# Optimization experiments

Measured on AMD Instinct MI355X. Metric: run time of the kernel, lower is better.

## Reference

```python
import jax, jax.numpy as jnp
import numpy as np
from jax import lax

K = 7          # k1 = k2
L1 = 8
L2 = 8
BLK = 8        # block_size
DIV = 4        # histogram bin-merge factor from extract_features_big_memory
DN = ('NCHW', 'OIHW', 'NCHW')
PAD = [(K // 2, K // 2), (K // 2, K // 2)]


def setup_inputs() -> dict:
    key = jax.random.key(0)
    k1, k2, k3 = jax.random.split(key, 3)
    x = jax.random.normal(k1, (32, 3, 128, 128), dtype=jnp.float32)
    w1 = jax.random.normal(k2, (L1, 3, K, K), dtype=jnp.float32)   # l1_conv weight
    w2 = jax.random.normal(k3, (L2, 1, K, K), dtype=jnp.float32)   # l2_conv weight
    return {"x": x, "w1": w1, "w2": w2}


def reference(x, w1, w2):
    # ----- two PCA-filter convolutions (same padding, stride 1, no bias) -----
    out1 = lax.conv_general_dilated(x, w1, (1, 1), PAD, dimension_numbers=DN)
    num, ch, w, h = out1.shape                      # ch == L1
    out2 = lax.conv_general_dilated(out1.reshape(num * ch, 1, w, h), w2,
                                    (1, 1), PAD, dimension_numbers=DN)
    out2 = out2.reshape(num, ch, L2, w, h)

    # ----- heaviside + bit-pack to decimal codes in [0, 2^L2) -----
    bits = (out2 > 0).astype(jnp.int32)             # (num, L1, L2, w, h)
    weights = (2 ** jnp.arange(L2, dtype=jnp.int32))[None, None, :, None, None]
    decimal = jnp.sum(bits * weights, axis=2)       # (num, L1, w, h) integer codes

    # ----- non-overlapping BLKxBLK blocks (step == BLK, exact tiling) -----
    nb_w, nb_h = w // BLK, h // BLK
    blocks = decimal.reshape(num, ch, nb_w, BLK, nb_h, BLK)
    blocks = blocks.transpose(0, 1, 2, 4, 3, 5).reshape(num, ch, nb_w * nb_h, BLK * BLK)

    # ----- per-block histogram with 2^L2 / DIV coarse bins (width DIV) -----
    n_bins = (2 ** L2) // DIV                        # 64
    bucket = blocks // DIV                           # (num, ch, nblocks, BLK*BLK)
    flat = bucket.reshape(-1, BLK * BLK)             # (N, 64 pixels)
    N = flat.shape[0]
    counts = jnp.zeros((N, n_bins), jnp.float32).at[
        jnp.arange(N)[:, None], flat].add(1.0)       # scatter-add histogram
    return counts.reshape(num, -1)                   # (num, L1*nblocks*n_bins)
```

## Files before the change

kernel.cpp:

```cpp
#include <hip/hip_runtime.h>
#include <hip/hip_bf16.h>

#define KK 7
#define NL1 8
#define NL2 8
#define IMG 128
#define REG 32
#define RT 38
#define O1P 40
#define XR 44
#define XTP 44
#define NBINS 64
#define NHB 16


#define LDX12(dst, plane, row, col)                                          \
    { float4 t_;                                                             \
      t_ = *(const float4*)&xt[plane][row][col];                             \
      dst[0]=t_.x; dst[1]=t_.y; dst[2]=t_.z; dst[3]=t_.w;                    \
      t_ = *(const float4*)&xt[plane][row][(col)+4];                         \
      dst[4]=t_.x; dst[5]=t_.y; dst[6]=t_.z; dst[7]=t_.w;                    \
      t_ = *(const float4*)&xt[plane][row][(col)+8];                         \
      dst[8]=t_.x; dst[9]=t_.y; dst[10]=t_.z; dst[11]=t_.w; }

#define C1TAPS(acc0, acc1, acc2, acc3, dp)                                   \
    _Pragma("unroll")                                                        \
    for (int dq = 0; dq < KK; ++dq) {                                        \
        float wa = w1g[(dp) * 7 + dq];                                       \
        float wb = w1g[49 + (dp) * 7 + dq];                                  \
        float wc = w1g[98 + (dp) * 7 + dq];                                  \
        acc0 = __builtin_fmaf(f0[dq + 0], wa, acc0);                         \
        acc0 = __builtin_fmaf(f1[dq + 0], wb, acc0);                         \
        acc0 = __builtin_fmaf(f2[dq + 0], wc, acc0);                         \
        acc1 = __builtin_fmaf(f0[dq + 1], wa, acc1);                         \
        acc1 = __builtin_fmaf(f1[dq + 1], wb, acc1);                         \
        acc1 = __builtin_fmaf(f2[dq + 1], wc, acc1);                         \
        acc2 = __builtin_fmaf(f0[dq + 2], wa, acc2);                         \
        acc2 = __builtin_fmaf(f1[dq + 2], wb, acc2);                         \
        acc2 = __builtin_fmaf(f2[dq + 2], wc, acc2);                         \
        acc3 = __builtin_fmaf(f0[dq + 3], wa, acc3);                         \
        acc3 = __builtin_fmaf(f1[dq + 3], wb, acc3);                         \
        acc3 = __builtin_fmaf(f2[dq + 3], wc, acc3);                         \
    }

__global__ __launch_bounds__(256, 5) void pcanet_fused(
    const float* __restrict__ x,
    const float* __restrict__ w1,
    const float* __restrict__ w2,
    float* __restrict__ out)
{
    const int tid = threadIdx.x;
    const int reg = blockIdx.x;
    const int ch  = blockIdx.y;
    const int n   = blockIdx.z;
    const int P0  = (reg >> 2) * REG;
    const int Q0  = (reg & 3) * REG;

    __shared__ __align__(16) float xt[3][XR][XTP];
    __shared__ __align__(16) float o1[RT][O1P];
    __shared__ unsigned int hist[NHB * 32];

    const float* __restrict__ w1g = w1 + ch * 147;
    const float* __restrict__ w2g = w2;

    {
        const int lane = tid & 63;
        const int wv   = tid >> 6;
        const float* xn = x + (size_t)n * 3 * IMG * IMG;
        const int gs = Q0 - 6 + lane;
        const bool cok = (gs >= 0) && (gs < IMG);
        if (lane < XTP) {
            for (int c = 0; c < 3; ++c)
                for (int r = wv; r < XR; r += 4) {
                    int gr = P0 - 6 + r;
                    float v = 0.0f;
                    if (cok && gr >= 0 && gr < IMG)
                        v = xn[((size_t)c * IMG + gr) * IMG + gs];
                    xt[c][r][lane] = v;
                }
        }
    }
    for (int i = tid; i < NHB * 32; i += 256) hist[i] = 0u;
    __syncthreads();

    if (tid < 190) {
        int pr = tid / 10;
        int c1 = 4 * (tid % 10);
        int r0 = 2 * pr;
        float a0 = 0.f, a1 = 0.f, a2 = 0.f, a3 = 0.f;
        float b0 = 0.f, b1 = 0.f, b2 = 0.f, b3 = 0.f;
        #pragma unroll
        for (int e = 0; e < 8; ++e) {
            float f0[12], f1[12], f2[12];
            LDX12(f0, 0, r0 + e, c1)
            LDX12(f1, 1, r0 + e, c1)
            LDX12(f2, 2, r0 + e, c1)
            if (e < 7) { C1TAPS(a0, a1, a2, a3, e) }
            if (e >= 1) { C1TAPS(b0, b1, b2, b3, e - 1) }
        }
        int gs0 = Q0 - 3 + c1;
        bool c0ok = (gs0 + 0 >= 0 && gs0 + 0 < IMG);
        bool c1ok = (gs0 + 1 >= 0 && gs0 + 1 < IMG);
        bool c2ok = (gs0 + 2 >= 0 && gs0 + 2 < IMG);
        bool c3ok = (gs0 + 3 >= 0 && gs0 + 3 < IMG);
        {
            int gr = P0 - 3 + r0;
            bool rok = (gr >= 0 && gr < IMG);
            float4 st;
            st.x = (rok && c0ok) ? a0 : 0.f;
            st.y = (rok && c1ok) ? a1 : 0.f;
            st.z = (rok && c2ok) ? a2 : 0.f;
            st.w = (rok && c3ok) ? a3 : 0.f;
            *(float4*)&o1[r0][c1] = st;
        }
        {
            int gr = P0 - 3 + r0 + 1;
            bool rok = (gr >= 0 && gr < IMG);
            float4 st;
            st.x = (rok && c0ok) ? b0 : 0.f;
            st.y = (rok && c1ok) ? b1 : 0.f;
            st.z = (rok && c2ok) ? b2 : 0.f;
            st.w = (rok && c3ok) ? b3 : 0.f;
            *(float4*)&o1[r0 + 1][c1] = st;
        }
    }
    __syncthreads();

    {
        const int r  = tid >> 3;
        const int c0 = (tid & 7) * 4;
        float acc[NL2][4];
        #pragma unroll
        for (int l = 0; l < NL2; ++l)
            #pragma unroll
            for (int k = 0; k < 4; ++k) acc[l][k] = 0.f;

        for (int dp = 0; dp < KK; ++dp) {
            float f[12];
            { float4 t_;
              t_ = *(const float4*)&o1[r + dp][c0];
              f[0]=t_.x; f[1]=t_.y; f[2]=t_.z; f[3]=t_.w;
              t_ = *(const float4*)&o1[r + dp][c0 + 4];
              f[4]=t_.x; f[5]=t_.y; f[6]=t_.z; f[7]=t_.w;
              t_ = *(const float4*)&o1[r + dp][c0 + 8];
              f[8]=t_.x; f[9]=t_.y; f[10]=t_.z; f[11]=t_.w; }
            #pragma unroll
            for (int l = 0; l < NL2; ++l)
                #pragma unroll
                for (int dq = 0; dq < KK; ++dq) {
                    float w = w2g[l * 49 + dp * 7 + dq];
                    acc[l][0] = __builtin_fmaf(f[dq + 0], w, acc[l][0]);
                    acc[l][1] = __builtin_fmaf(f[dq + 1], w, acc[l][1]);
                    acc[l][2] = __builtin_fmaf(f[dq + 2], w, acc[l][2]);
                    acc[l][3] = __builtin_fmaf(f[dq + 3], w, acc[l][3]);
                }
        }
        #pragma unroll
        for (int k = 0; k < 4; ++k) {
            int code = 0;
            #pragma unroll
            for (int l = 0; l < NL2; ++l)
                if (acc[l][k] > 0.0f) code |= (1 << l);
            int bin = code >> 2;
            int bc = (c0 + k) >> 3, br = r >> 3;
            atomicAdd(&hist[(br * 4 + bc) * 32 + (bin >> 1)],
                      1u << (16 * (bin & 1)));
        }
    }
    __syncthreads();

    size_t planeBase = ((size_t)(n * NL1 + ch)) * 256 * NBINS;
    for (int i = tid; i < NHB * NBINS; i += 256) {
        int bl = i >> 6, bin = i & 63;
        unsigned int w = hist[bl * 32 + (bin >> 1)];
        unsigned int cnt = (w >> (16 * (bin & 1))) & 0xFFFFu;
        int br = bl >> 2, bc = bl & 3;
        int blkg = ((P0 >> 3) + br) * 16 + ((Q0 >> 3) + bc);
        out[planeBase + (size_t)blkg * NBINS + bin] = (float)cnt;
    }
}

extern "C" void kernel_launch(void* const* d_in, const int* in_sizes, int n_in,
                              void* d_out, int out_size, void* d_ws, size_t ws_size,
                              hipStream_t stream) {
    const float* x  = (const float*)d_in[0];
    const float* w1 = (const float*)d_in[1];
    const float* w2 = (const float*)d_in[2];
    float* out = (float*)d_out;

    dim3 grid(16, NL1, 32);
    dim3 block(256);
    pcanet_fused<<<grid, block, 0, stream>>>(x, w1, w2, out);
}
```

Measured before the change: 82.15 us.

## Make each wave compute its own conv1 stripe and histogram blocks, removing block barriers

The block is split so each wavefront computes the conv1 rows it needs for its own 8-row stripe, including the halo, then runs conv2 and its own 4 histogram blocks. This removes the two block-wide __syncthreads that separated the conv1, conv2 and histogram stages. In exchange, conv1 halo rows are computed redundantly by neighbouring waves. Each wave now runs two passes of conv1 tasks, and the second pass leaves most lanes idle.

New measurement: 113.5 us. +38.2%, slower.

```diff
diff --git a/kernel.cpp b/kernel.cpp
--- a/kernel.cpp
+++ b/kernel.cpp
@@ -49,7 +49,9 @@
     const float* __restrict__ w2,
     float* __restrict__ out)
 {
-    const int tid = threadIdx.x;
+    const int tid  = threadIdx.x;
+    const int wave = tid >> 6;
+    const int lane = tid & 63;
     const int reg = blockIdx.x;
     const int ch  = blockIdx.y;
     const int n   = blockIdx.z;
@@ -64,14 +66,12 @@
     const float* __restrict__ w2g = w2;
 
     {
-        const int lane = tid & 63;
-        const int wv   = tid >> 6;
         const float* xn = x + (size_t)n * 3 * IMG * IMG;
         const int gs = Q0 - 6 + lane;
         const bool cok = (gs >= 0) && (gs < IMG);
         if (lane < XTP) {
             for (int c = 0; c < 3; ++c)
-                for (int r = wv; r < XR; r += 4) {
+                for (int r = wave; r < XR; r += 4) {
                     int gr = P0 - 6 + r;
                     float v = 0.0f;
                     if (cok && gr >= 0 && gr < IMG)
@@ -80,55 +80,59 @@
                 }
         }
     }
-    for (int i = tid; i < NHB * 32; i += 256) hist[i] = 0u;
+    hist[wave * 128 + lane]      = 0u;
+    hist[wave * 128 + 64 + lane] = 0u;
     __syncthreads();
 
-    if (tid < 190) {
-        int pr = tid / 10;
-        int c1 = 4 * (tid % 10);
-        int r0 = 2 * pr;
-        float a0 = 0.f, a1 = 0.f, a2 = 0.f, a3 = 0.f;
-        float b0 = 0.f, b1 = 0.f, b2 = 0.f, b3 = 0.f;
-        #pragma unroll
-        for (int e = 0; e < 8; ++e) {
-            float f0[12], f1[12], f2[12];
-            LDX12(f0, 0, r0 + e, c1)
-            LDX12(f1, 1, r0 + e, c1)
-            LDX12(f2, 2, r0 + e, c1)
-            if (e < 7) { C1TAPS(a0, a1, a2, a3, e) }
-            if (e >= 1) { C1TAPS(b0, b1, b2, b3, e - 1) }
-        }
-        int gs0 = Q0 - 3 + c1;
-        bool c0ok = (gs0 + 0 >= 0 && gs0 + 0 < IMG);
-        bool c1ok = (gs0 + 1 >= 0 && gs0 + 1 < IMG);
-        bool c2ok = (gs0 + 2 >= 0 && gs0 + 2 < IMG);
-        bool c3ok = (gs0 + 3 >= 0 && gs0 + 3 < IMG);
-        {
-            int gr = P0 - 3 + r0;
-            bool rok = (gr >= 0 && gr < IMG);
-            float4 st;
-            st.x = (rok && c0ok) ? a0 : 0.f;
-            st.y = (rok && c1ok) ? a1 : 0.f;
-            st.z = (rok && c2ok) ? a2 : 0.f;
-            st.w = (rok && c3ok) ? a3 : 0.f;
-            *(float4*)&o1[r0][c1] = st;
-        }
-        {
-            int gr = P0 - 3 + r0 + 1;
-            bool rok = (gr >= 0 && gr < IMG);
-            float4 st;
-            st.x = (rok && c0ok) ? b0 : 0.f;
-            st.y = (rok && c1ok) ? b1 : 0.f;
-            st.z = (rok && c2ok) ? b2 : 0.f;
-            st.w = (rok && c3ok) ? b3 : 0.f;
-            *(float4*)&o1[r0 + 1][c1] = st;
+    #pragma unroll
+    for (int t = 0; t < 2; ++t) {
+        int task = lane + (t << 6);
+        if (task < 70) {
+            int pr = task / 10;
+            int c1 = 4 * (task % 10);
+            int r0 = (wave << 3) + 2 * pr;
+            float a0 = 0.f, a1 = 0.f, a2 = 0.f, a3 = 0.f;
+            float b0 = 0.f, b1 = 0.f, b2 = 0.f, b3 = 0.f;
+            #pragma unroll
+            for (int e = 0; e < 8; ++e) {
+                float f0[12], f1[12], f2[12];
+                LDX12(f0, 0, r0 + e, c1)
+                LDX12(f1, 1, r0 + e, c1)
+                LDX12(f2, 2, r0 + e, c1)
+                if (e < 7)  { C1TAPS(a0, a1, a2, a3, e) }
+                if (e >= 1) { C1TAPS(b0, b1, b2, b3, e - 1) }
+            }
+            int gs0 = Q0 - 3 + c1;
+            bool c0ok = (gs0 + 0 >= 0 && gs0 + 0 < IMG);
+            bool c1ok = (gs0 + 1 >= 0 && gs0 + 1 < IMG);
+            bool c2ok = (gs0 + 2 >= 0 && gs0 + 2 < IMG);
+            bool c3ok = (gs0 + 3 >= 0 && gs0 + 3 < IMG);
+            {
+                int gr = P0 - 3 + r0;
+                bool rok = (gr >= 0 && gr < IMG);
+                float4 st;
+                st.x = (rok && c0ok) ? a0 : 0.f;
+                st.y = (rok && c1ok) ? a1 : 0.f;
+                st.z = (rok && c2ok) ? a2 : 0.f;
+                st.w = (rok && c3ok) ? a3 : 0.f;
+                *(float4*)&o1[r0][c1] = st;
+            }
+            {
+                int gr = P0 - 3 + r0 + 1;
+                bool rok = (gr >= 0 && gr < IMG);
+                float4 st;
+                st.x = (rok && c0ok) ? b0 : 0.f;
+                st.y = (rok && c1ok) ? b1 : 0.f;
+                st.z = (rok && c2ok) ? b2 : 0.f;
+                st.w = (rok && c3ok) ? b3 : 0.f;
+                *(float4*)&o1[r0 + 1][c1] = st;
+            }
         }
     }
-    __syncthreads();
 
     {
-        const int r  = tid >> 3;
-        const int c0 = (tid & 7) * 4;
+        const int r  = (wave << 3) + (lane >> 3);
+        const int c0 = (lane & 7) * 4;
         float acc[NL2][4];
         #pragma unroll
         for (int l = 0; l < NL2; ++l)
@@ -162,16 +166,16 @@
             for (int l = 0; l < NL2; ++l)
                 if (acc[l][k] > 0.0f) code |= (1 << l);
             int bin = code >> 2;
-            int bc = (c0 + k) >> 3, br = r >> 3;
-            atomicAdd(&hist[(br * 4 + bc) * 32 + (bin >> 1)],
+            int blkid = (wave << 2) + ((c0 + k) >> 3);
+            atomicAdd(&hist[blkid * 32 + (bin >> 1)],
                       1u << (16 * (bin & 1)));
         }
     }
-    __syncthreads();
 
     size_t planeBase = ((size_t)(n * NL1 + ch)) * 256 * NBINS;
-    for (int i = tid; i < NHB * NBINS; i += 256) {
-        int bl = i >> 6, bin = i & 63;
+    for (int i = lane; i < 4 * NBINS; i += 64) {
+        int bl = (wave << 2) + (i >> 6);
+        int bin = i & 63;
         unsigned int w = hist[bl * 32 + (bin >> 1)];
         unsigned int cnt = (w >> (16 * (bin & 1))) & 0xFFFFu;
         int br = bl >> 2, bc = bl & 3;
```

## Split fused kernel into conv1-to-workspace and conv2-histogram kernels

Applied to the files above, without the earlier changes.

Replaces the single fused kernel with two launches when workspace allows. The first computes all 8 first-stage channels per tile once and writes them to global memory. The second reads one channel's halo tile from that buffer and does conv2 and the histogram. This removes the halo recompute and the 8x redundant conv1 work across channel blocks, at the cost of a 16MB global round trip and an extra launch. The old fused path is kept as a fallback.

Result: slower. 272.1 us (+231.2%).

```diff
diff --git a/kernel.cpp b/kernel.cpp
--- a/kernel.cpp
+++ b/kernel.cpp
@@ -23,29 +23,77 @@
       t_ = *(const float4*)&xt[plane][row][(col)+8];                         \
       dst[8]=t_.x; dst[9]=t_.y; dst[10]=t_.z; dst[11]=t_.w; }
 
-#define C1TAPS(acc0, acc1, acc2, acc3, dp)                                   \
-    _Pragma("unroll")                                                        \
-    for (int dq = 0; dq < KK; ++dq) {                                        \
-        float wa = w1g[(dp) * 7 + dq];                                       \
-        float wb = w1g[49 + (dp) * 7 + dq];                                  \
-        float wc = w1g[98 + (dp) * 7 + dq];                                  \
-        acc0 = __builtin_fmaf(f0[dq + 0], wa, acc0);                         \
-        acc0 = __builtin_fmaf(f1[dq + 0], wb, acc0);                         \
-        acc0 = __builtin_fmaf(f2[dq + 0], wc, acc0);                         \
-        acc1 = __builtin_fmaf(f0[dq + 1], wa, acc1);                         \
-        acc1 = __builtin_fmaf(f1[dq + 1], wb, acc1);                         \
-        acc1 = __builtin_fmaf(f2[dq + 1], wc, acc1);                         \
-        acc2 = __builtin_fmaf(f0[dq + 2], wa, acc2);                         \
-        acc2 = __builtin_fmaf(f1[dq + 2], wb, acc2);                         \
-        acc2 = __builtin_fmaf(f2[dq + 2], wc, acc2);                         \
-        acc3 = __builtin_fmaf(f0[dq + 3], wa, acc3);                         \
-        acc3 = __builtin_fmaf(f1[dq + 3], wb, acc3);                         \
-        acc3 = __builtin_fmaf(f2[dq + 3], wc, acc3);                         \
-    }
-
-__global__ __launch_bounds__(256, 5) void pcanet_fused(
+__global__ __launch_bounds__(256, 2) void pcanet_conv1(
     const float* __restrict__ x,
     const float* __restrict__ w1,
+    float* __restrict__ o1g)
+{
+    const int tid = threadIdx.x;
+    const int reg = blockIdx.x;
+    const int n   = blockIdx.y;
+    const int P0  = (reg >> 2) * REG;
+    const int Q0  = (reg & 3) * REG;
+
+    __shared__ __align__(16) float xt[3][RT][O1P];
+
+    {
+        const int lane = tid & 63, wv = tid >> 6;
+        const float* xn = x + (size_t)n * 3 * IMG * IMG;
+        const int gc = Q0 - 3 + lane;
+        const bool cok = (gc >= 0 && gc < IMG);
+        if (lane < O1P) {
+            for (int c = 0; c < 3; ++c)
+                for (int r = wv; r < RT; r += 4) {
+                    int gr = P0 - 3 + r;
+                    float v = 0.f;
+                    if (cok && gr >= 0 && gr < IMG)
+                        v = xn[((size_t)c * IMG + gr) * IMG + gc];
+                    xt[c][r][lane] = v;
+                }
+        }
+    }
+    __syncthreads();
+
+    const int row = tid >> 3;
+    const int c1  = (tid & 7) * 4;
+    float acc[NL1][4];
+    #pragma unroll
+    for (int ch = 0; ch < NL1; ++ch)
+        #pragma unroll
+        for (int k = 0; k < 4; ++k) acc[ch][k] = 0.f;
+
+    #pragma unroll
+    for (int e = 0; e < KK; ++e) {
+        float f0[12], f1[12], f2[12];
+        LDX12(f0, 0, row + e, c1)
+        LDX12(f1, 1, row + e, c1)
+        LDX12(f2, 2, row + e, c1)
+        #pragma unroll
+        for (int ch = 0; ch < NL1; ++ch)
+            #pragma unroll
+            for (int dq = 0; dq < KK; ++dq) {
+                const float wa = w1[ch * 147 +      e * 7 + dq];
+                const float wb = w1[ch * 147 + 49 + e * 7 + dq];
+                const float wc = w1[ch * 147 + 98 + e * 7 + dq];
+                #pragma unroll
+                for (int k = 0; k < 4; ++k) {
+                    acc[ch][k] = __builtin_fmaf(f0[dq + k], wa, acc[ch][k]);
+                    acc[ch][k] = __builtin_fmaf(f1[dq + k], wb, acc[ch][k]);
+                    acc[ch][k] = __builtin_fmaf(f2[dq + k], wc, acc[ch][k]);
+                }
+            }
+    }
+    const int gr = P0 + row, gc = Q0 + c1;
+    #pragma unroll
+    for (int ch = 0; ch < NL1; ++ch) {
+        float4 st;
+        st.x = acc[ch][0]; st.y = acc[ch][1]; st.z = acc[ch][2]; st.w = acc[ch][3];
+        *(float4*)&o1g[(((size_t)n * NL1 + ch) * IMG + gr) * IMG + gc] = st;
+    }
+}
+
+__global__ __launch_bounds__(256, 8) void pcanet_conv2(
+    const float* __restrict__ o1g,
     const float* __restrict__ w2,
     float* __restrict__ out)
 {
@@ -56,6 +104,123 @@
     const int P0  = (reg >> 2) * REG;
     const int Q0  = (reg & 3) * REG;
 
+    __shared__ __align__(16) float o1[RT][O1P];
+    __shared__ unsigned int hist[NHB * 32];
+
+    const float* __restrict__ w2g = w2;
+
+    {
+        const int lane = tid & 63, wv = tid >> 6;
+        const float* src = o1g + ((size_t)n * NL1 + ch) * IMG * IMG;
+        const int gc = Q0 - 3 + lane;
+        const bool cok = (gc >= 0 && gc < IMG);
+        if (lane < O1P) {
+            for (int r = wv; r < RT; r += 4) {
+                int gr = P0 - 3 + r;
+                float v = 0.f;
+                if (cok && gr >= 0 && gr < IMG)
+                    v = src[(size_t)gr * IMG + gc];
+                o1[r][lane] = v;
+            }
+        }
+    }
+    for (int i = tid; i < NHB * 32; i += 256) hist[i] = 0u;
+    __syncthreads();
+
+    {
+        const int r  = tid >> 3;
+        const int c0 = (tid & 7) * 4;
+        float acc[NL2][4];
+        #pragma unroll
+        for (int l = 0; l < NL2; ++l)
+            #pragma unroll
+            for (int k = 0; k < 4; ++k) acc[l][k] = 0.f;
+
+        for (int dp = 0; dp < KK; ++dp) {
+            float f[12];
+            { float4 t_;
+              t_ = *(const float4*)&o1[r + dp][c0];
+              f[0]=t_.x; f[1]=t_.y; f[2]=t_.z; f[3]=t_.w;
+              t_ = *(const float4*)&o1[r + dp][c0 + 4];
+              f[4]=t_.x; f[5]=t_.y; f[6]=t_.z; f[7]=t_.w;
+              t_ = *(const float4*)&o1[r + dp][c0 + 8];
+              f[8]=t_.x; f[9]=t_.y; f[10]=t_.z; f[11]=t_.w; }
+            #pragma unroll
+            for (int l = 0; l < NL2; ++l)
+                #pragma unroll
+                for (int dq = 0; dq < KK; ++dq) {
+                    float w = w2g[l * 49 + dp * 7 + dq];
+                    acc[l][0] = __builtin_fmaf(f[dq + 0], w, acc[l][0]);
+                    acc[l][1] = __builtin_fmaf(f[dq + 1], w, acc[l][1]);
+                    acc[l][2] = __builtin_fmaf(f[dq + 2], w, acc[l][2]);
+                    acc[l][3] = __builtin_fmaf(f[dq + 3], w, acc[l][3]);
+                }
+        }
+        #pragma unroll
+        for (int k = 0; k < 4; ++k) {
+            int code = 0;
+            #pragma unroll
+            for (int l = 0; l < NL2; ++l)
+                if (acc[l][k] > 0.0f) code |= (1 << l);
+            int bin = code >> 2;
+            int bc = (c0 + k) >> 3, br = r >> 3;
+            atomicAdd(&hist[(br * 4 + bc) * 32 + (bin >> 1)],
+                      1u << (16 * (bin & 1)));
+        }
+    }
+    __syncthreads();
+
+    size_t planeBase = ((size_t)(n * NL1 + ch)) * 256 * NBINS;
+    for (int i = tid; i < NHB * NBINS; i += 256) {
+        int bl = i >> 6, bin = i & 63;
+        unsigned int w = hist[bl * 32 + (bin >> 1)];
+        unsigned int cnt = (w >> (16 * (bin & 1))) & 0xFFFFu;
+        int br = bl >> 2, bc = bl & 3;
+        int blkg = ((P0 >> 3) + br) * 16 + ((Q0 >> 3) + bc);
+        out[planeBase + (size_t)blkg * NBINS + bin] = (float)cnt;
+    }
+}
+
+#define C1TAPS(acc0, acc1, acc2, acc3, dp)                                   \
+    _Pragma("unroll")                                                        \
+    for (int dq = 0; dq < KK; ++dq) {                                        \
+        float wa = w1g[(dp) * 7 + dq];                                       \
+        float wb = w1g[49 + (dp) * 7 + dq];                                  \
+        float wc = w1g[98 + (dp) * 7 + dq];                                  \
+        acc0 = __builtin_fmaf(fx0[dq + 0], wa, acc0);                        \
+        acc0 = __builtin_fmaf(fx1[dq + 0], wb, acc0);                        \
+        acc0 = __builtin_fmaf(fx2[dq + 0], wc, acc0);                        \
+        acc1 = __builtin_fmaf(fx0[dq + 1], wa, acc1);                        \
+        acc1 = __builtin_fmaf(fx1[dq + 1], wb, acc1);                        \
+        acc1 = __builtin_fmaf(fx2[dq + 1], wc, acc1);                        \
+        acc2 = __builtin_fmaf(fx0[dq + 2], wa, acc2);                        \
+        acc2 = __builtin_fmaf(fx1[dq + 2], wb, acc2);                        \
+        acc2 = __builtin_fmaf(fx2[dq + 2], wc, acc2);                        \
+        acc3 = __builtin_fmaf(fx0[dq + 3], wa, acc3);                        \
+        acc3 = __builtin_fmaf(fx1[dq + 3], wb, acc3);                        \
+        acc3 = __builtin_fmaf(fx2[dq + 3], wc, acc3);                        \
+    }
+
+#define LDXF(dst, plane, rw, col)                                            \
+    { float4 t_;                                                             \
+      t_ = *(const float4*)&xt[plane][rw][col];                              \
+      dst[0]=t_.x; dst[1]=t_.y; dst[2]=t_.z; dst[3]=t_.w;                    \
+      t_ = *(const float4*)&xt[plane][rw][(col)+4];                          \
+      dst[4]=t_.x; dst[5]=t_.y; dst[6]=t_.z; dst[7]=t_.w;                    \
+      t_ = *(const float4*)&xt[plane][rw][(col)+8];                          \
+      dst[8]=t_.x; dst[9]=t_.y; dst[10]=t_.z; dst[11]=t_.w; }
+
+__global__ __launch_bounds__(256, 5) void pcanet_fused(
+    const float* __restrict__ x, const float* __restrict__ w1,
+    const float* __restrict__ w2, float* __restrict__ out)
+{
+    const int tid = threadIdx.x;
+    const int reg = blockIdx.x;
+    const int ch  = blockIdx.y;
+    const int n   = blockIdx.z;
+    const int P0  = (reg >> 2) * REG;
+    const int Q0  = (reg & 3) * REG;
+
     __shared__ __align__(16) float xt[3][XR][XTP];
     __shared__ __align__(16) float o1[RT][O1P];
     __shared__ unsigned int hist[NHB * 32];
@@ -64,8 +229,7 @@
     const float* __restrict__ w2g = w2;
 
     {
-        const int lane = tid & 63;
-        const int wv   = tid >> 6;
+        const int lane = tid & 63, wv = tid >> 6;
         const float* xn = x + (size_t)n * 3 * IMG * IMG;
         const int gs = Q0 - 6 + lane;
         const bool cok = (gs >= 0) && (gs < IMG);
@@ -84,18 +248,16 @@
     __syncthreads();
 
     if (tid < 190) {
-        int pr = tid / 10;
-        int c1 = 4 * (tid % 10);
-        int r0 = 2 * pr;
+        int pr = tid / 10, c1 = 4 * (tid % 10), r0 = 2 * pr;
         float a0 = 0.f, a1 = 0.f, a2 = 0.f, a3 = 0.f;
         float b0 = 0.f, b1 = 0.f, b2 = 0.f, b3 = 0.f;
         #pragma unroll
         for (int e = 0; e < 8; ++e) {
-            float f0[12], f1[12], f2[12];
-            LDX12(f0, 0, r0 + e, c1)
-            LDX12(f1, 1, r0 + e, c1)
-            LDX12(f2, 2, r0 + e, c1)
-            if (e < 7) { C1TAPS(a0, a1, a2, a3, e) }
+            float fx0[12], fx1[12], fx2[12];
+            LDXF(fx0, 0, r0 + e, c1)
+            LDXF(fx1, 1, r0 + e, c1)
+            LDXF(fx2, 2, r0 + e, c1)
+            if (e < 7)  { C1TAPS(a0, a1, a2, a3, e) }
             if (e >= 1) { C1TAPS(b0, b1, b2, b3, e - 1) }
         }
         int gs0 = Q0 - 3 + c1;
@@ -107,20 +269,16 @@
             int gr = P0 - 3 + r0;
             bool rok = (gr >= 0 && gr < IMG);
             float4 st;
-            st.x = (rok && c0ok) ? a0 : 0.f;
-            st.y = (rok && c1ok) ? a1 : 0.f;
-            st.z = (rok && c2ok) ? a2 : 0.f;
-            st.w = (rok && c3ok) ? a3 : 0.f;
+            st.x = (rok && c0ok) ? a0 : 0.f; st.y = (rok && c1ok) ? a1 : 0.f;
+            st.z = (rok && c2ok) ? a2 : 0.f; st.w = (rok && c3ok) ? a3 : 0.f;
             *(float4*)&o1[r0][c1] = st;
         }
         {
             int gr = P0 - 3 + r0 + 1;
             bool rok = (gr >= 0 && gr < IMG);
             float4 st;
-            st.x = (rok && c0ok) ? b0 : 0.f;
-            st.y = (rok && c1ok) ? b1 : 0.f;
-            st.z = (rok && c2ok) ? b2 : 0.f;
-            st.w = (rok && c3ok) ? b3 : 0.f;
+            st.x = (rok && c0ok) ? b0 : 0.f; st.y = (rok && c1ok) ? b1 : 0.f;
+            st.z = (rok && c2ok) ? b2 : 0.f; st.w = (rok && c3ok) ? b3 : 0.f;
             *(float4*)&o1[r0 + 1][c1] = st;
         }
     }
@@ -188,7 +346,12 @@
     const float* w2 = (const float*)d_in[2];
     float* out = (float*)d_out;
 
-    dim3 grid(16, NL1, 32);
-    dim3 block(256);
-    pcanet_fused<<<grid, block, 0, stream>>>(x, w1, w2, out);
+    const size_t need = (size_t)32 * NL1 * IMG * IMG * sizeof(float);
+    if (ws_size >= need) {
+        float* o1g = (float*)d_ws;
+        pcanet_conv1<<<dim3(16, 32),      256, 0, stream>>>(x, w1, o1g);
+        pcanet_conv2<<<dim3(16, NL1, 32), 256, 0, stream>>>(o1g, w2, out);
+    } else {
+        pcanet_fused<<<dim3(16, NL1, 32), 256, 0, stream>>>(x, w1, w2, out);
+    }
 }
```
